# Optimization experiments

Measured on AMD Instinct MI355X. Metric: run time of the kernel, lower is better.

The kernel has to match this reference:

```python
import jax, jax.numpy as jnp
import numpy as np
import math

K = 8
MOMENTUM = 0.999


def _gelu(x):
    c = math.sqrt(2.0 / math.pi)
    return 0.5 * x * (1.0 + jnp.tanh(c * (x + 0.044715 * x ** 3)))


def _normalize(v, eps=1e-12):
    n = jnp.linalg.norm(v, axis=-1, keepdims=True)
    return v / jnp.maximum(n, eps)


def setup_inputs() -> dict:
    key = jax.random.key(0)
    k1, k2 = jax.random.split(key)
    B, T, D = 4, 4096, 2048
    x = jax.random.normal(k1, (B, T, D), dtype=jnp.float32)
    prototypes = _normalize(jax.random.normal(k2, (K, D), dtype=jnp.float32))
    log_tau = jnp.asarray(math.log(2.0), dtype=jnp.float32)
    log_blend = jnp.asarray(math.log(0.3 / 0.7), dtype=jnp.float32)
    return {"x": x, "prototypes": prototypes, "log_tau": log_tau, "log_blend": log_blend}


def reference(x, prototypes, log_tau, log_blend):
    tau = jnp.exp(log_tau)
    alpha = jax.nn.sigmoid(log_blend)
    B, T, D = x.shape
    x_flat = jax.lax.stop_gradient(x.reshape(-1, D))  # [N, D], detached

    P_norm = _normalize(prototypes)                  # [K, D]
    xn = _normalize(x_flat, eps=1e-8)                # [N, D]

    sims = jnp.clip(xn @ P_norm.T, -1.0, 1.0)        # [N, K]
    assignments = jnp.argmax(sims, axis=-1)          # [N]

    # masked per-cluster mean via segment-sum (vectorized over K)
    sums = jax.ops.segment_sum(x_flat, assignments, num_segments=K)       # [K, D]
    counts = jax.ops.segment_sum(jnp.ones((x_flat.shape[0],), x.dtype),
                                 assignments, num_segments=K)             # [K]
    has = (counts > 0)[:, None]
    centroids = jnp.where(has, sums / jnp.maximum(counts, 1.0)[:, None], prototypes)
    new_P = _normalize(centroids)

    P2 = MOMENTUM * prototypes + (1.0 - MOMENTUM) * new_P
    P2n = _normalize(P2, eps=1e-8)

    sims2 = jnp.clip(xn @ P2n.T, -1.0, 1.0)          # [N, K]
    dists = jnp.clip(1.0 - jnp.max(sims2, axis=-1), 0.0, 2.0)
    novelty = (1.0 - jnp.exp(-tau * dists)).reshape(B, T)

    scale = jnp.clip(1.0 - alpha + alpha * novelty[..., None], 0.1, 10.0)
    return _gelu(x * scale)
```

## Files before the change

kernel.cpp:

```cpp
#include <hip/hip_runtime.h>

#define N_TOK 16384
#define DDIM  2048
#define KC    8
#define CH1   32

typedef float nfloat4 __attribute__((ext_vector_type(4)));

__device__ __forceinline__ void nt_store4(const float4& v, float* p){
  nfloat4 nv; nv.x = v.x; nv.y = v.y; nv.z = v.z; nv.w = v.w;
  __builtin_nontemporal_store(nv, (nfloat4*)p);
}
__device__ __forceinline__ float4 nt_load4(const float* p){
  nfloat4 nv = __builtin_nontemporal_load((const nfloat4*)p);
  return make_float4(nv.x, nv.y, nv.z, nv.w);
}

__device__ __forceinline__ float wave_sum(float v){
  #pragma unroll
  for (int off = 32; off > 0; off >>= 1)
    v += __shfl_xor(v, off, 64);
  return v;
}

__device__ __forceinline__ float gelu_tanh(float v){
  const float c = 0.7978845608028654f;
  float tt = c * v * (1.0f + 0.044715f * v * v);
  float e  = __expf(2.0f * tt);
  float th = 1.0f - 2.0f / (e + 1.0f);
  return 0.5f * v * (1.0f + th);
}

__global__ __launch_bounds__(256, 2)
void k_assign(const float* __restrict__ x, const float* __restrict__ proto,
              float* __restrict__ psums, float* __restrict__ pcnts, int ntok)
{
  const int t = threadIdx.x;
  const int wave = t >> 6, lane = t & 63;
  const int d0 = 4*t, d1 = DDIM/2 + 4*t;

  __shared__ float red[4*KC];
  __shared__ float sInv[KC];
  __shared__ float sCnt[KC];
  __shared__ int   sA;

  float4 P0[KC], P1[KC];
  float4 acc0[KC], acc1[KC];
  #pragma unroll
  for (int k = 0; k < KC; ++k){
    P0[k] = *(const float4*)(proto + k*DDIM + d0);
    P1[k] = *(const float4*)(proto + k*DDIM + d1);
    acc0[k] = make_float4(0.f,0.f,0.f,0.f);
    acc1[k] = make_float4(0.f,0.f,0.f,0.f);
  }
  if (t < KC) sCnt[t] = 0.f;

  #pragma unroll
  for (int k = 0; k < KC; ++k){
    float ss = P0[k].x*P0[k].x + P0[k].y*P0[k].y + P0[k].z*P0[k].z + P0[k].w*P0[k].w
             + P1[k].x*P1[k].x + P1[k].y*P1[k].y + P1[k].z*P1[k].z + P1[k].w*P1[k].w;
    ss = wave_sum(ss);
    if (lane == 0) red[wave*KC + k] = ss;
  }
  __syncthreads();
  if (t < KC){
    float ss = red[t] + red[KC + t] + red[2*KC + t] + red[3*KC + t];
    sInv[t] = 1.0f / fmaxf(sqrtf(ss), 1e-12f);
  }
  __syncthreads();
  float invP[KC];
  #pragma unroll
  for (int k = 0; k < KC; ++k) invP[k] = sInv[k];

  int tok = blockIdx.x;
  float4 nx0 = make_float4(0,0,0,0), nx1 = make_float4(0,0,0,0);
  if (tok < ntok){
    nx0 = *(const float4*)(x + (size_t)tok*DDIM + d0);
    nx1 = *(const float4*)(x + (size_t)tok*DDIM + d1);
  }
  for (; tok < ntok; tok += gridDim.x){
    float4 cx0 = nx0, cx1 = nx1;
    int nt = tok + gridDim.x;
    if (nt < ntok){
      nx0 = *(const float4*)(x + (size_t)nt*DDIM + d0);
      nx1 = *(const float4*)(x + (size_t)nt*DDIM + d1);
    }
    float dot[KC];
    #pragma unroll
    for (int k = 0; k < KC; ++k){
      float dv = cx0.x*P0[k].x + cx0.y*P0[k].y + cx0.z*P0[k].z + cx0.w*P0[k].w
               + cx1.x*P1[k].x + cx1.y*P1[k].y + cx1.z*P1[k].z + cx1.w*P1[k].w;
      dot[k] = wave_sum(dv);
    }
    if (lane == 0){
      #pragma unroll
      for (int k = 0; k < KC; ++k) red[wave*KC + k] = dot[k];
    }
    __syncthreads();
    if (t == 0){
      int best = 0; float bv = -3.4e38f;
      #pragma unroll
      for (int k = 0; k < KC; ++k){
        float v = (red[k] + red[KC+k] + red[2*KC+k] + red[3*KC+k]) * invP[k];
        if (v > bv){ bv = v; best = k; }
      }
      sA = best;
      sCnt[best] += 1.0f;
    }
    __syncthreads();
    const int a = sA;
    #pragma unroll
    for (int k = 0; k < KC; ++k){
      if (a == k){
        acc0[k].x += cx0.x; acc0[k].y += cx0.y; acc0[k].z += cx0.z; acc0[k].w += cx0.w;
        acc1[k].x += cx1.x; acc1[k].y += cx1.y; acc1[k].z += cx1.z; acc1[k].w += cx1.w;
      }
    }
  }
  __syncthreads();
  float* dst = psums + (size_t)blockIdx.x * (KC*DDIM);
  #pragma unroll
  for (int k = 0; k < KC; ++k){
    nt_store4(acc0[k], dst + k*DDIM + d0);
    nt_store4(acc1[k], dst + k*DDIM + d1);
  }
  if (t < KC) pcnts[blockIdx.x*KC + t] = sCnt[t];
}

__global__ __launch_bounds__(256)
void k_reduce1(const float* __restrict__ psums, const float* __restrict__ pcnts,
               float* __restrict__ stage2, float* __restrict__ cnt2, int nb, int cs)
{
  const int ch = blockIdx.x >> 4;
  const int g  = blockIdx.x & 15;
  const int col = g*1024 + threadIdx.x*4;
  const int b0 = ch*cs;

  float4 acc = make_float4(0.f,0.f,0.f,0.f);
  #pragma unroll 4
  for (int i = 0; i < cs; ++i){
    int b = b0 + i;
    if (b < nb){
      float4 v = nt_load4(psums + (size_t)b*(KC*DDIM) + col);
      acc.x += v.x; acc.y += v.y; acc.z += v.z; acc.w += v.w;
    }
  }
  *(float4*)(stage2 + (size_t)ch*(KC*DDIM) + col) = acc;

  if (g == 0 && threadIdx.x < KC){
    float c = 0.f;
    for (int i = 0; i < cs; ++i){
      int b = b0 + i;
      if (b < nb) c += pcnts[b*KC + threadIdx.x];
    }
    cnt2[ch*KC + threadIdx.x] = c;
  }
}

__global__ __launch_bounds__(256)
void k_reduce2(const float* __restrict__ stage2, const float* __restrict__ cnt2,
               const float* __restrict__ proto, float* __restrict__ centroid)
{
  __shared__ float cnt[KC];
  if (threadIdx.x < KC){
    float c = 0.f;
    #pragma unroll
    for (int ch = 0; ch < CH1; ++ch) c += cnt2[ch*KC + threadIdx.x];
    cnt[threadIdx.x] = c;
  }
  __syncthreads();
  const int col = blockIdx.x*1024 + threadIdx.x*4;
  float4 s = make_float4(0.f,0.f,0.f,0.f);
  #pragma unroll
  for (int ch = 0; ch < CH1; ++ch){
    float4 v = *(const float4*)(stage2 + (size_t)ch*(KC*DDIM) + col);
    s.x += v.x; s.y += v.y; s.z += v.z; s.w += v.w;
  }
  const int k = col >> 11;
  const float c = cnt[k];
  float4 o;
  if (c > 0.f){
    float inv = 1.0f / fmaxf(c, 1.f);
    o.x = s.x*inv; o.y = s.y*inv; o.z = s.z*inv; o.w = s.w*inv;
  } else {
    o = *(const float4*)(proto + col);
  }
  *(float4*)(centroid + col) = o;
}

__global__ void k_pupdate(const float* __restrict__ centroid, const float* __restrict__ proto,
                          float* __restrict__ p2n)
{
  const int t = threadIdx.x;
  const int w = t >> 6, lane = t & 63;
  float4 c[8], pr[8];
  float ss = 0.f;
  #pragma unroll
  for (int j = 0; j < 8; ++j){
    const int d = (j*64 + lane)*4;
    c[j]  = *(const float4*)(centroid + w*DDIM + d);
    pr[j] = *(const float4*)(proto    + w*DDIM + d);
    ss += c[j].x*c[j].x + c[j].y*c[j].y + c[j].z*c[j].z + c[j].w*c[j].w;
  }
  ss = wave_sum(ss);
  const float invc = 1.0f / fmaxf(sqrtf(ss), 1e-12f);
  const float m = 0.999f, om = 1.0f - 0.999f;
  float4 p2[8];
  float ss2 = 0.f;
  #pragma unroll
  for (int j = 0; j < 8; ++j){
    p2[j].x = m*pr[j].x + om*c[j].x*invc;
    p2[j].y = m*pr[j].y + om*c[j].y*invc;
    p2[j].z = m*pr[j].z + om*c[j].z*invc;
    p2[j].w = m*pr[j].w + om*c[j].w*invc;
    ss2 += p2[j].x*p2[j].x + p2[j].y*p2[j].y + p2[j].z*p2[j].z + p2[j].w*p2[j].w;
  }
  ss2 = wave_sum(ss2);
  const float inv2 = 1.0f / fmaxf(sqrtf(ss2), 1e-8f);
  #pragma unroll
  for (int j = 0; j < 8; ++j){
    const int d = (j*64 + lane)*4;
    float4 o;
    o.x = p2[j].x*inv2; o.y = p2[j].y*inv2; o.z = p2[j].z*inv2; o.w = p2[j].w*inv2;
    *(float4*)(p2n + w*DDIM + d) = o;
  }
}

__global__ __launch_bounds__(256, 2)
void k_final(const float* __restrict__ x, const float* __restrict__ p2n,
             const float* __restrict__ plog_tau, const float* __restrict__ plog_blend,
             float* __restrict__ out, int ntok)
{
  const int t = threadIdx.x;
  const int wave = t >> 6, lane = t & 63;
  const int d0 = 4*t, d1 = DDIM/2 + 4*t;

  __shared__ float red[4*(KC+1)];
  __shared__ float sScale;

  float4 P0[KC], P1[KC];
  #pragma unroll
  for (int k = 0; k < KC; ++k){
    P0[k] = *(const float4*)(p2n + k*DDIM + d0);
    P1[k] = *(const float4*)(p2n + k*DDIM + d1);
  }
  const float tau   = __expf(plog_tau[0]);
  const float alpha = 1.0f / (1.0f + __expf(-plog_blend[0]));

  int tok = blockIdx.x;
  float4 nx0 = make_float4(0,0,0,0), nx1 = make_float4(0,0,0,0);
  if (tok < ntok){
    nx0 = *(const float4*)(x + (size_t)tok*DDIM + d0);
    nx1 = *(const float4*)(x + (size_t)tok*DDIM + d1);
  }
  for (; tok < ntok; tok += gridDim.x){
    float4 cx0 = nx0, cx1 = nx1;
    int nt = tok + gridDim.x;
    if (nt < ntok){
      nx0 = *(const float4*)(x + (size_t)nt*DDIM + d0);
      nx1 = *(const float4*)(x + (size_t)nt*DDIM + d1);
    }
    float ss = cx0.x*cx0.x + cx0.y*cx0.y + cx0.z*cx0.z + cx0.w*cx0.w
             + cx1.x*cx1.x + cx1.y*cx1.y + cx1.z*cx1.z + cx1.w*cx1.w;
    ss = wave_sum(ss);
    float dot[KC];
    #pragma unroll
    for (int k = 0; k < KC; ++k){
      float dv = cx0.x*P0[k].x + cx0.y*P0[k].y + cx0.z*P0[k].z + cx0.w*P0[k].w
               + cx1.x*P1[k].x + cx1.y*P1[k].y + cx1.z*P1[k].z + cx1.w*P1[k].w;
      dot[k] = wave_sum(dv);
    }
    if (lane == 0){
      #pragma unroll
      for (int k = 0; k < KC; ++k) red[wave*(KC+1) + k] = dot[k];
      red[wave*(KC+1) + KC] = ss;
    }
    __syncthreads();
    if (t == 0){
      float fss = red[KC] + red[(KC+1)+KC] + red[2*(KC+1)+KC] + red[3*(KC+1)+KC];
      float inv = 1.0f / fmaxf(sqrtf(fss), 1e-8f);
      float mx = -3.4e38f;
      #pragma unroll
      for (int k = 0; k < KC; ++k){
        float v = red[k] + red[(KC+1)+k] + red[2*(KC+1)+k] + red[3*(KC+1)+k];
        mx = fmaxf(mx, v);
      }
      float s    = fminf(fmaxf(mx * inv, -1.0f), 1.0f);
      float dist = fminf(fmaxf(1.0f - s, 0.0f), 2.0f);
      float nov  = 1.0f - __expf(-tau * dist);
      float sc   = 1.0f - alpha + alpha * nov;
      sScale = fminf(fmaxf(sc, 0.1f), 10.0f);
    }
    __syncthreads();
    const float sc = sScale;
    float* o = out + (size_t)tok*DDIM;
    float4 o0, o1;
    o0.x = gelu_tanh(cx0.x*sc); o0.y = gelu_tanh(cx0.y*sc);
    o0.z = gelu_tanh(cx0.z*sc); o0.w = gelu_tanh(cx0.w*sc);
    o1.x = gelu_tanh(cx1.x*sc); o1.y = gelu_tanh(cx1.y*sc);
    o1.z = gelu_tanh(cx1.z*sc); o1.w = gelu_tanh(cx1.w*sc);
    nt_store4(o0, o + d0);
    nt_store4(o1, o + d1);
  }
}

extern "C" void kernel_launch(void* const* d_in, const int* in_sizes, int n_in,
                              void* d_out, int out_size, void* d_ws, size_t ws_size,
                              hipStream_t stream)
{
  const float* x          = (const float*)d_in[0];
  const float* proto      = (const float*)d_in[1];
  const float* log_tau    = (const float*)d_in[2];
  const float* log_blend  = (const float*)d_in[3];
  float* out = (float*)d_out;
  float* ws  = (float*)d_ws;

  const int ntok = in_sizes[0] / DDIM;

  float* centroid = ws;
  float* p2n      = ws + 16384;
  float* pcnts    = ws + 32768;
  float* cnt2     = ws + 36864;
  float* stage2   = ws + 37120;
  float* psums    = ws + 37120 + CH1*KC*DDIM;

  long cap = (long)(ws_size / 4) - (37120 + CH1*KC*DDIM);
  int nb = (int)(cap / (KC * DDIM));
  if (nb > 512) nb = 512;
  if (nb < 1)  nb = 1;
  const int cs = (nb + CH1 - 1) / CH1;

  k_assign <<<nb,      256, 0, stream>>>(x, proto, psums, pcnts, ntok);
  k_reduce1<<<CH1*16,  256, 0, stream>>>(psums, pcnts, stage2, cnt2, nb, cs);
  k_reduce2<<<16,      256, 0, stream>>>(stage2, cnt2, proto, centroid);
  k_pupdate<<<1,       512, 0, stream>>>(centroid, proto, p2n);
  k_final  <<<512,     256, 0, stream>>>(x, p2n, log_tau, log_blend, out, ntok);
}
```

Measured before the change: 353.3 us.

## Batch four tokens per block iteration and use transpose-butterfly reductions

Both the assignment and final kernels now process TBA/TBF=4 tokens per loop iteration instead of one, which spreads the two block barriers and the serial single-thread argmax over four tokens. The eight per-prototype wave reductions are replaced by a butterfly transpose-reduce, so each lane ends up holding a different k and far fewer shuffles are needed. Each block also keeps more x loads in flight through a four-token prefetch. The cost is higher register pressure, since there are now 16 float4 buffers of x on top of the prototype and accumulator registers. Under launch_bounds(256,2) that could cause spills, particularly in k_assign.

New measurement: 306.8 us. 13.2% less time.

```diff
diff --git a/kernel.cpp b/kernel.cpp
--- a/kernel.cpp
+++ b/kernel.cpp
@@ -4,6 +4,8 @@
 #define DDIM  2048
 #define KC    8
 #define CH1   32
+#define TBA   4
+#define TBF   4
 
 typedef float nfloat4 __attribute__((ext_vector_type(4)));
 
@@ -21,6 +23,37 @@
   for (int off = 32; off > 0; off >>= 1)
     v += __shfl_xor(v, off, 64);
   return v;
+}
+
+__device__ __forceinline__ float butterfly8(float v[8], int t){
+  {
+    const bool h = (t & 1);
+    #pragma unroll
+    for (int j = 0; j < 4; ++j){
+      float s    = h ? v[j]   : v[j+4];
+      float keep = h ? v[j+4] : v[j];
+      v[j] = keep + __shfl_xor(s, 1, 64);
+    }
+  }
+  {
+    const bool h = (t & 2);
+    #pragma unroll
+    for (int j = 0; j < 2; ++j){
+      float s    = h ? v[j]   : v[j+2];
+      float keep = h ? v[j+2] : v[j];
+      v[j] = keep + __shfl_xor(s, 2, 64);
+    }
+  }
+  {
+    const bool h = (t & 4);
+    float s    = h ? v[0] : v[1];
+    float keep = h ? v[1] : v[0];
+    v[0] = keep + __shfl_xor(s, 4, 64);
+  }
+  v[0] += __shfl_xor(v[0], 8, 64);
+  v[0] += __shfl_xor(v[0], 16, 64);
+  v[0] += __shfl_xor(v[0], 32, 64);
+  return v[0];
 }
 
 __device__ __forceinline__ float gelu_tanh(float v){
@@ -38,11 +71,13 @@
   const int t = threadIdx.x;
   const int wave = t >> 6, lane = t & 63;
   const int d0 = 4*t, d1 = DDIM/2 + 4*t;
-
-  __shared__ float red[4*KC];
+  const int kidx = ((lane&1)<<2) | (lane&2) | ((lane>>2)&1);
+
+  __shared__ float rednorm[4*KC];
+  __shared__ float red[TBA][4][KC];
   __shared__ float sInv[KC];
   __shared__ float sCnt[KC];
-  __shared__ int   sA;
+  __shared__ int   sAsg[TBA];
 
   float4 P0[KC], P1[KC];
   float4 acc0[KC], acc1[KC];
@@ -60,62 +95,77 @@
     float ss = P0[k].x*P0[k].x + P0[k].y*P0[k].y + P0[k].z*P0[k].z + P0[k].w*P0[k].w
              + P1[k].x*P1[k].x + P1[k].y*P1[k].y + P1[k].z*P1[k].z + P1[k].w*P1[k].w;
     ss = wave_sum(ss);
-    if (lane == 0) red[wave*KC + k] = ss;
+    if (lane == 0) rednorm[wave*KC + k] = ss;
   }
   __syncthreads();
   if (t < KC){
-    float ss = red[t] + red[KC + t] + red[2*KC + t] + red[3*KC + t];
+    float ss = rednorm[t] + rednorm[KC + t] + rednorm[2*KC + t] + rednorm[3*KC + t];
     sInv[t] = 1.0f / fmaxf(sqrtf(ss), 1e-12f);
   }
   __syncthreads();
-  float invP[KC];
-  #pragma unroll
-  for (int k = 0; k < KC; ++k) invP[k] = sInv[k];
-
-  int tok = blockIdx.x;
-  float4 nx0 = make_float4(0,0,0,0), nx1 = make_float4(0,0,0,0);
-  if (tok < ntok){
-    nx0 = *(const float4*)(x + (size_t)tok*DDIM + d0);
-    nx1 = *(const float4*)(x + (size_t)tok*DDIM + d1);
-  }
-  for (; tok < ntok; tok += gridDim.x){
-    float4 cx0 = nx0, cx1 = nx1;
-    int nt = tok + gridDim.x;
-    if (nt < ntok){
-      nx0 = *(const float4*)(x + (size_t)nt*DDIM + d0);
-      nx1 = *(const float4*)(x + (size_t)nt*DDIM + d1);
-    }
-    float dot[KC];
-    #pragma unroll
-    for (int k = 0; k < KC; ++k){
-      float dv = cx0.x*P0[k].x + cx0.y*P0[k].y + cx0.z*P0[k].z + cx0.w*P0[k].w
-               + cx1.x*P1[k].x + cx1.y*P1[k].y + cx1.z*P1[k].z + cx1.w*P1[k].w;
-      dot[k] = wave_sum(dv);
-    }
-    if (lane == 0){
+
+  const int stride = gridDim.x * TBA;
+  float4 X0[TBA], X1[TBA], N0[TBA], N1[TBA];
+  int tok0 = blockIdx.x * TBA;
+  #pragma unroll
+  for (int i = 0; i < TBA; ++i){
+    int tk = tok0 + i;
+    X0[i] = make_float4(0,0,0,0); X1[i] = make_float4(0,0,0,0);
+    if (tk < ntok){
+      X0[i] = *(const float4*)(x + (size_t)tk*DDIM + d0);
+      X1[i] = *(const float4*)(x + (size_t)tk*DDIM + d1);
+    }
+  }
+
+  for (; tok0 < ntok; tok0 += stride){
+    const int ntok0 = tok0 + stride;
+    #pragma unroll
+    for (int i = 0; i < TBA; ++i){
+      int tk = ntok0 + i;
+      N0[i] = make_float4(0,0,0,0); N1[i] = make_float4(0,0,0,0);
+      if (tk < ntok){
+        N0[i] = *(const float4*)(x + (size_t)tk*DDIM + d0);
+        N1[i] = *(const float4*)(x + (size_t)tk*DDIM + d1);
+      }
+    }
+    #pragma unroll
+    for (int i = 0; i < TBA; ++i){
+      float v[KC];
       #pragma unroll
-      for (int k = 0; k < KC; ++k) red[wave*KC + k] = dot[k];
+      for (int k = 0; k < KC; ++k){
+        v[k] = X0[i].x*P0[k].x + X0[i].y*P0[k].y + X0[i].z*P0[k].z + X0[i].w*P0[k].w
+             + X1[i].x*P1[k].x + X1[i].y*P1[k].y + X1[i].z*P1[k].z + X1[i].w*P1[k].w;
+      }
+      float r = butterfly8(v, t);
+      if (lane < 8) red[i][wave][kidx] = r;
     }
     __syncthreads();
-    if (t == 0){
+    if (t < TBA && tok0 + t < ntok){
       int best = 0; float bv = -3.4e38f;
       #pragma unroll
       for (int k = 0; k < KC; ++k){
-        float v = (red[k] + red[KC+k] + red[2*KC+k] + red[3*KC+k]) * invP[k];
-        if (v > bv){ bv = v; best = k; }
-      }
-      sA = best;
-      sCnt[best] += 1.0f;
+        float val = (red[t][0][k] + red[t][1][k] + red[t][2][k] + red[t][3][k]) * sInv[k];
+        if (val > bv){ bv = val; best = k; }
+      }
+      sAsg[t] = best;
+      atomicAdd(&sCnt[best], 1.0f);
     }
     __syncthreads();
-    const int a = sA;
-    #pragma unroll
-    for (int k = 0; k < KC; ++k){
-      if (a == k){
-        acc0[k].x += cx0.x; acc0[k].y += cx0.y; acc0[k].z += cx0.z; acc0[k].w += cx0.w;
-        acc1[k].x += cx1.x; acc1[k].y += cx1.y; acc1[k].z += cx1.z; acc1[k].w += cx1.w;
-      }
-    }
+    #pragma unroll
+    for (int i = 0; i < TBA; ++i){
+      if (tok0 + i < ntok){
+        const int a = sAsg[i];
+        #pragma unroll
+        for (int k = 0; k < KC; ++k){
+          if (a == k){
+            acc0[k].x += X0[i].x; acc0[k].y += X0[i].y; acc0[k].z += X0[i].z; acc0[k].w += X0[i].w;
+            acc1[k].x += X1[i].x; acc1[k].y += X1[i].y; acc1[k].z += X1[i].z; acc1[k].w += X1[i].w;
+          }
+        }
+      }
+    }
+    #pragma unroll
+    for (int i = 0; i < TBA; ++i){ X0[i] = N0[i]; X1[i] = N1[i]; }
   }
   __syncthreads();
   float* dst = psums + (size_t)blockIdx.x * (KC*DDIM);
@@ -234,9 +284,11 @@
   const int t = threadIdx.x;
   const int wave = t >> 6, lane = t & 63;
   const int d0 = 4*t, d1 = DDIM/2 + 4*t;
-
-  __shared__ float red[4*(KC+1)];
-  __shared__ float sScale;
+  const int kidx = ((lane&1)<<2) | (lane&2) | ((lane>>2)&1);
+
+  __shared__ float red[TBF][4][KC];
+  __shared__ float redss[TBF][4];
+  __shared__ float sScale[TBF];
 
   float4 P0[KC], P1[KC];
   #pragma unroll
@@ -247,60 +299,79 @@
   const float tau   = __expf(plog_tau[0]);
   const float alpha = 1.0f / (1.0f + __expf(-plog_blend[0]));
 
-  int tok = blockIdx.x;
-  float4 nx0 = make_float4(0,0,0,0), nx1 = make_float4(0,0,0,0);
-  if (tok < ntok){
-    nx0 = *(const float4*)(x + (size_t)tok*DDIM + d0);
-    nx1 = *(const float4*)(x + (size_t)tok*DDIM + d1);
-  }
-  for (; tok < ntok; tok += gridDim.x){
-    float4 cx0 = nx0, cx1 = nx1;
-    int nt = tok + gridDim.x;
-    if (nt < ntok){
-      nx0 = *(const float4*)(x + (size_t)nt*DDIM + d0);
-      nx1 = *(const float4*)(x + (size_t)nt*DDIM + d1);
-    }
-    float ss = cx0.x*cx0.x + cx0.y*cx0.y + cx0.z*cx0.z + cx0.w*cx0.w
-             + cx1.x*cx1.x + cx1.y*cx1.y + cx1.z*cx1.z + cx1.w*cx1.w;
-    ss = wave_sum(ss);
-    float dot[KC];
-    #pragma unroll
-    for (int k = 0; k < KC; ++k){
-      float dv = cx0.x*P0[k].x + cx0.y*P0[k].y + cx0.z*P0[k].z + cx0.w*P0[k].w
-               + cx1.x*P1[k].x + cx1.y*P1[k].y + cx1.z*P1[k].z + cx1.w*P1[k].w;
-      dot[k] = wave_sum(dv);
-    }
-    if (lane == 0){
+  const int stride = gridDim.x * TBF;
+  float4 X0[TBF], X1[TBF], N0[TBF], N1[TBF];
+  int tok0 = blockIdx.x * TBF;
+  #pragma unroll
+  for (int i = 0; i < TBF; ++i){
+    int tk = tok0 + i;
+    X0[i] = make_float4(0,0,0,0); X1[i] = make_float4(0,0,0,0);
+    if (tk < ntok){
+      X0[i] = *(const float4*)(x + (size_t)tk*DDIM + d0);
+      X1[i] = *(const float4*)(x + (size_t)tk*DDIM + d1);
+    }
+  }
+
+  for (; tok0 < ntok; tok0 += stride){
+    const int ntok0 = tok0 + stride;
+    #pragma unroll
+    for (int i = 0; i < TBF; ++i){
+      int tk = ntok0 + i;
+      N0[i] = make_float4(0,0,0,0); N1[i] = make_float4(0,0,0,0);
+      if (tk < ntok){
+        N0[i] = *(const float4*)(x + (size_t)tk*DDIM + d0);
+        N1[i] = *(const float4*)(x + (size_t)tk*DDIM + d1);
+      }
+    }
+    #pragma unroll
+    for (int i = 0; i < TBF; ++i){
+      float v[KC];
       #pragma unroll
-      for (int k = 0; k < KC; ++k) red[wave*(KC+1) + k] = dot[k];
-      red[wave*(KC+1) + KC] = ss;
+      for (int k = 0; k < KC; ++k){
+        v[k] = X0[i].x*P0[k].x + X0[i].y*P0[k].y + X0[i].z*P0[k].z + X0[i].w*P0[k].w
+             + X1[i].x*P1[k].x + X1[i].y*P1[k].y + X1[i].z*P1[k].z + X1[i].w*P1[k].w;
+      }
+      float r = butterfly8(v, t);
+      if (lane < 8) red[i][wave][kidx] = r;
+      float ss = X0[i].x*X0[i].x + X0[i].y*X0[i].y + X0[i].z*X0[i].z + X0[i].w*X0[i].w
+               + X1[i].x*X1[i].x + X1[i].y*X1[i].y + X1[i].z*X1[i].z + X1[i].w*X1[i].w;
+      ss = wave_sum(ss);
+      if (lane == 0) redss[i][wave] = ss;
     }
     __syncthreads();
-    if (t == 0){
-      float fss = red[KC] + red[(KC+1)+KC] + red[2*(KC+1)+KC] + red[3*(KC+1)+KC];
+    if (t < TBF && tok0 + t < ntok){
+      float fss = redss[t][0] + redss[t][1] + redss[t][2] + redss[t][3];
       float inv = 1.0f / fmaxf(sqrtf(fss), 1e-8f);
       float mx = -3.4e38f;
       #pragma unroll
       for (int k = 0; k < KC; ++k){
-        float v = red[k] + red[(KC+1)+k] + red[2*(KC+1)+k] + red[3*(KC+1)+k];
-        mx = fmaxf(mx, v);
+        float val = red[t][0][k] + red[t][1][k] + red[t][2][k] + red[t][3][k];
+        mx = fmaxf(mx, val);
       }
       float s    = fminf(fmaxf(mx * inv, -1.0f), 1.0f);
       float dist = fminf(fmaxf(1.0f - s, 0.0f), 2.0f);
       float nov  = 1.0f - __expf(-tau * dist);
       float sc   = 1.0f - alpha + alpha * nov;
-      sScale = fminf(fmaxf(sc, 0.1f), 10.0f);
+      sScale[t]  = fminf(fmaxf(sc, 0.1f), 10.0f);
     }
     __syncthreads();
-    const float sc = sScale;
-    float* o = out + (size_t)tok*DDIM;
-    float4 o0, o1;
-    o0.x = gelu_tanh(cx0.x*sc); o0.y = gelu_tanh(cx0.y*sc);
-    o0.z = gelu_tanh(cx0.z*sc); o0.w = gelu_tanh(cx0.w*sc);
-    o1.x = gelu_tanh(cx1.x*sc); o1.y = gelu_tanh(cx1.y*sc);
-    o1.z = gelu_tanh(cx1.z*sc); o1.w = gelu_tanh(cx1.w*sc);
-    nt_store4(o0, o + d0);
-    nt_store4(o1, o + d1);
+    #pragma unroll
+    for (int i = 0; i < TBF; ++i){
+      int tk = tok0 + i;
+      if (tk < ntok){
+        const float sc = sScale[i];
+        float* o = out + (size_t)tk*DDIM;
+        float4 o0, o1;
+        o0.x = gelu_tanh(X0[i].x*sc); o0.y = gelu_tanh(X0[i].y*sc);
+        o0.z = gelu_tanh(X0[i].z*sc); o0.w = gelu_tanh(X0[i].w*sc);
+        o1.x = gelu_tanh(X1[i].x*sc); o1.y = gelu_tanh(X1[i].y*sc);
+        o1.z = gelu_tanh(X1[i].z*sc); o1.w = gelu_tanh(X1[i].w*sc);
+        nt_store4(o0, o + d0);
+        nt_store4(o1, o + d1);
+      }
+    }
+    #pragma unroll
+    for (int i = 0; i < TBF; ++i){ X0[i] = N0[i]; X1[i] = N1[i]; }
   }
 }
 
```
